# Optimization experiments

Measured on AMD Instinct MI355X. Metric: run time of the kernel, lower is better.

Reference implementation:

```python
import jax, jax.numpy as jnp
import numpy as np

EPS = 1e-6  # mmdet bbox_overlaps eps


def _nearest_bev(boxes7):
    # boxes7: [N, 7] = (x, y, z, dx, dy, dz, yaw). LiDARInstance3DBoxes.nearest_bev:
    # limit yaw to [-pi/2, pi/2) via limit_period(yaw, 0.5, pi); if |yaw| > pi/4 swap dx/dy,
    # then return axis-aligned (x1, y1, x2, y2).
    x, y = boxes7[:, 0], boxes7[:, 1]
    dx, dy = boxes7[:, 3], boxes7[:, 4]
    yaw = boxes7[:, 6]
    pi = jnp.float32(np.pi)
    normed = jnp.abs(yaw - jnp.floor(yaw / pi + 0.5) * pi)
    swap = normed > pi / 4
    w = jnp.where(swap, dy, dx)
    h = jnp.where(swap, dx, dy)
    return jnp.stack([x - w / 2, y - h / 2, x + w / 2, y + h / 2], axis=-1)


def _pairwise_iou(b):
    # b: [N, 4] x1y1x2y2 -> [N, N] IoU (mmdet bbox_overlaps, mode='iou')
    area = (b[:, 2] - b[:, 0]) * (b[:, 3] - b[:, 1])
    lt = jnp.maximum(b[:, None, :2], b[None, :, :2])
    rb = jnp.minimum(b[:, None, 2:], b[None, :, 2:])
    wh = jnp.clip(rb - lt, 0.0)
    inter = wh[..., 0] * wh[..., 1]
    union = jnp.maximum(area[:, None] + area[None, :] - inter, EPS)
    return inter / union


def setup_inputs() -> dict:
    key = jax.random.key(0)
    k1, k2, k3, k4, k5, k6 = jax.random.split(key, 6)
    B, A, C, H, W, box_dim = 2, 2, 10, 32, 32, 7
    N = H * W * A
    scores = jax.random.normal(k1, (B, A * C, H, W), jnp.float32)
    bbox_preds = jax.random.normal(k2, (B, A * box_dim, H, W), jnp.float32)
    pp_params = jax.random.normal(k3, (B, C * 3, H, W), jnp.float32)
    centers = jax.random.uniform(k4, (B, N, 3), jnp.float32, 0.0, 50.0)
    sizes = jax.random.uniform(k5, (B, N, 3), jnp.float32, 1.0, 5.0)
    yaw = jax.random.uniform(k6, (B, N, 1), jnp.float32, -np.pi, np.pi)
    decoded = jnp.concatenate([centers, sizes, yaw], axis=-1)  # [B, N, 7]
    return {"scores": scores, "bbox_preds": bbox_preds, "pp_params": pp_params, "decoded": decoded}


def reference(scores, bbox_preds, pp_params, decoded):
    B, AC, H, W = scores.shape
    N = decoded.shape[1]
    A = N // (H * W)
    C = AC // A
    # flatten_scores: (B,A,C,H,W) -> (B,H,W,A,C) -> (B, HWA, C)
    sc_f = scores.reshape(B, A, C, H, W).transpose(0, 3, 4, 1, 2).reshape(B, N, C)
    # flatten_pp: (B,C,3,H,W) -> (B,H,W,C,3), broadcast over A -> (B, HWA, C, 3)
    pp_hw = pp_params.reshape(B, C, 3, H, W).transpose(0, 3, 4, 1, 2)  # [B,H,W,C,3]
    pp_f = jnp.broadcast_to(pp_hw[:, :, :, None, :, :], (B, H, W, A, C, 3)).reshape(B, N, C, 3)
    # per-batch BEV IoU matrices
    bev = jax.vmap(_nearest_bev)(decoded[..., :7])        # [B, N, 4]
    iou = jax.vmap(_pairwise_iou)(bev)                    # [B, N, N]
    # per-class outer-product bias + row softmax + matmul with column softmax of scores
    p0 = pp_f[..., 0]                                     # [B, N, C]
    p1 = pp_f[..., 1]                                     # [B, N, C]
    bias = p0[:, :, None, :] * p1[:, None, :, :]          # [B, N, N, C]
    weight = jax.nn.softmax(iou[..., None] + bias, axis=2)  # softmax over keys (dim=1 of NxN)
    sm_sc = jax.nn.softmax(sc_f, axis=1)                  # softmax over N per class
    new_sc = jnp.einsum('bnmc,bmc->bnc', weight, sm_sc)   # [B, N, C]
    # un-flatten back to level layout: (B,H,W,A,C) -> (B, A*C, H, W)
    out_scores = new_sc.reshape(B, H, W, A, C).transpose(0, 3, 4, 1, 2).reshape(B, A * C, H, W)
    return out_scores, bbox_preds, pp_params
```

## Files before the change

### kernel.cpp

```cpp
#include <hip/hip_runtime.h>
#include <math.h>

#define Bz 2
#define Az 2
#define Cz 10
#define HWz 1024
#define Nz 2048
#define ACHW (Az*Cz*HWz)
#define NBBOX (Bz*Az*7*HWz)
#define NPP   (Bz*Cz*3*HWz)
#define EPSf 1e-6f
#define LOG2E 1.4426950408889634f

#if __has_builtin(__builtin_amdgcn_exp2f)
#define EXP2F(x) __builtin_amdgcn_exp2f(x)
#else
#define EXP2F(x) exp2f(x)
#endif
#if __has_builtin(__builtin_amdgcn_rcpf)
#define RCPF(x) __builtin_amdgcn_rcpf(x)
#else
#define RCPF(x) (1.0f/(x))
#endif

static __device__ __forceinline__ unsigned short f2bf(float x) {
    unsigned u = __builtin_bit_cast(unsigned, x);
    unsigned r = (u + 0x7fffu + ((u >> 16) & 1u)) >> 16;
    return (unsigned short)r;
}

#if __has_builtin(__builtin_amdgcn_update_dpp)
static __device__ __forceinline__ float wred(float x) {
    int t;
    t = __builtin_amdgcn_update_dpp(0, __builtin_bit_cast(int, x), 0x111, 0xf, 0xf, true);
    x += __builtin_bit_cast(float, t);
    t = __builtin_amdgcn_update_dpp(0, __builtin_bit_cast(int, x), 0x112, 0xf, 0xf, true);
    x += __builtin_bit_cast(float, t);
    t = __builtin_amdgcn_update_dpp(0, __builtin_bit_cast(int, x), 0x114, 0xf, 0xf, true);
    x += __builtin_bit_cast(float, t);
    t = __builtin_amdgcn_update_dpp(0, __builtin_bit_cast(int, x), 0x118, 0xf, 0xf, true);
    x += __builtin_bit_cast(float, t);
    t = __builtin_amdgcn_update_dpp(0, __builtin_bit_cast(int, x), 0x142, 0xa, 0xf, true);
    x += __builtin_bit_cast(float, t);
    t = __builtin_amdgcn_update_dpp(0, __builtin_bit_cast(int, x), 0x143, 0xc, 0xf, true);
    x += __builtin_bit_cast(float, t);
    return x;
}
#define WRED_LANE 63
#else
static __device__ __forceinline__ float wred(float x) {
    for (int off = 32; off > 0; off >>= 1) x += __shfl_down(x, off);
    return x;
}
#define WRED_LANE 0
#endif

static __device__ __forceinline__ float iou_e(float nx1,float ny1,float nx2,float ny2,float ar,
                                              float mx1,float my1,float mx2,float my2,float am) {
    float xx1 = fmaxf(nx1, mx1), yy1 = fmaxf(ny1, my1);
    float xx2 = fminf(nx2, mx2), yy2 = fminf(ny2, my2);
    float iw = fmaxf(xx2 - xx1, 0.f), ih = fmaxf(yy2 - yy1, 0.f);
    float inter = iw * ih;
    float uni = fmaxf(ar + am - inter, EPSf);
    return EXP2F(inter * LOG2E * RCPF(uni));
}

#define GL16(g, l) __builtin_amdgcn_global_load_lds( \
    (const __attribute__((address_space(1))) void*)(g), \
    (__attribute__((address_space(3))) void*)(l), 16, 0, 0)


__global__ __launch_bounds__(256) void k_pre(const float* __restrict__ scores,
                                             const float* __restrict__ bbox,
                                             const float* __restrict__ pp,
                                             const float* __restrict__ dec,
                                             float* __restrict__ out,
                                             float2* __restrict__ LT,
                                             float2* __restrict__ RB,
                                             uint2* __restrict__ GPQ) {
    int blk = blockIdx.x;
    int tid = threadIdx.x;

    if (blk < 240) {
        int i = blk * 256 + tid;
        if (i < NBBOX) out[Bz*ACHW + i] = bbox[i];
        if (i < NPP)   out[Bz*ACHW + NBBOX + i] = pp[i];
        return;
    }
    if (blk < 256) {
        int i = (blk - 240) * 256 + tid;
        const float* d = dec + i*7;
        float x = d[0], y = d[1], dx = d[3], dy = d[4], yaw = d[6];
        const float PI = 3.14159265358979323846f;
        float normed = fabsf(yaw - floorf(yaw/PI + 0.5f) * PI);
        bool swp = normed > PI * 0.25f;
        float w = swp ? dy : dx;
        float h = swp ? dx : dy;
        LT[i] = make_float2(x - 0.5f*w, y - 0.5f*h);
        RB[i] = make_float2(x + 0.5f*w, y + 0.5f*h);
        return;
    }
    __shared__ float wr4[4], ws4[4];
    __shared__ float SV[Nz];
    int wave = tid >> 6, lane = tid & 63;
    int bc = blk - 256;
    int b = bc / Cz, c = bc % Cz;
    const float* sbase = scores + b*ACHW;
    float vals[Nz/256];
    float mx = -INFINITY;
    #pragma unroll
    for (int j = 0; j < Nz/256; j++) {
        int n = tid + (j << 8);
        int a = n & 1, hw = n >> 1;
        float v = sbase[(a*Cz + c)*HWz + hw];
        vals[j] = v;
        mx = fmaxf(mx, v);
    }
    #pragma unroll
    for (int off = 32; off > 0; off >>= 1) mx = fmaxf(mx, __shfl_xor(mx, off));
    if (lane == 0) wr4[wave] = mx;
    __syncthreads();
    mx = fmaxf(fmaxf(wr4[0], wr4[1]), fmaxf(wr4[2], wr4[3]));
    float sum = 0.f;
    #pragma unroll
    for (int j = 0; j < Nz/256; j++) {
        float e = EXP2F((vals[j] - mx) * LOG2E);
        sum += e;
        SV[tid + (j << 8)] = e;
    }
    #pragma unroll
    for (int off = 32; off > 0; off >>= 1) sum += __shfl_xor(sum, off);
    if (lane == 0) ws4[wave] = sum;
    __syncthreads();
    float inv = 1.f / (ws4[0] + ws4[1] + ws4[2] + ws4[3]);
    const float* p1base = pp + b*Cz*3*HWz + (c*3 + 1)*HWz;
    uint2* gp = GPQ + (b*Cz + c)*HWz;
    #pragma unroll
    for (int k = 0; k < 4; k++) {
        int hm = tid + (k << 8);
        float q0 = SV[2*hm] * inv, q1 = SV[2*hm + 1] * inv;
        unsigned qq = (unsigned)f2bf(q0) | ((unsigned)f2bf(q1) << 16);
        float p1 = p1base[hm] * LOG2E;
        gp[hm] = make_uint2(__builtin_bit_cast(unsigned, p1), qq);
    }
}

__global__ __launch_bounds__(256, 4) void k_main(const float4* __restrict__ LT4,
                                                 const float4* __restrict__ RB4,
                                                 const uint2* __restrict__ GPQ,
                                                 const float* __restrict__ pp,
                                                 float* __restrict__ out) {
    __shared__ __align__(16) float4 SBuf[2][2][128];
    __shared__ __align__(16) uint2  SQb[2][2][640];
    __shared__ float SRED[2][2][40];

    int tid = threadIdx.x;
    int wave = tid >> 6, lane = tid & 63;
    int hl = wave >> 1;
    int s  = wave & 1;
    int bid = blockIdx.x;
    int b = bid >> 9;
    int g = bid & 511;
    int hn = (g << 1) + hl;
    int mb = s << 9;

    const float4* LTb = LT4 + (b << 10);
    const float4* RBb = RB4 + (b << 10);
    const uint2*  PQb = GPQ + b * (Cz * HWz);

    float4 bx = LTb[hn];
    float4 by = RBb[hn];
    float ar0 = (by.x - bx.x) * (by.y - bx.y);
    float ar1 = (by.z - bx.z) * (by.w - bx.w);

    float p0[Cz];
    const float* p0base = pp + b*(Cz*3*HWz) + hn;
    #pragma unroll
    for (int c = 0; c < Cz; c++) p0[c] = p0base[c * 3 * HWz];

    float l0[Cz], l1[Cz], a0[Cz], a1[Cz];
    #pragma unroll
    for (int c = 0; c < Cz; c++) { l0[c]=0.f; l1[c]=0.f; a0[c]=0.f; a1[c]=0.f; }

    auto stage = [&](int nb, int t) {
        int hbase = mb + (t << 6);
        if (hl) {
            GL16(LTb + hbase + lane, &SBuf[nb][s][0]);
            GL16(RBb + hbase + lane, &SBuf[nb][s][64]);
        } else {
            #pragma unroll
            for (int k = 0; k < 5; k++) {
                int p = (k << 6) + lane;
                int c = p >> 5;
                int hml2 = (p & 31) << 1;
                GL16(PQb + (c << 10) + hbase + hml2, &SQb[nb][s][k << 7]);
            }
        }
    };

    stage(0, 0);
    for (int it = 0; it < 8; ++it) {
        __syncthreads();
        int cur = it & 1;
        if (it < 7) stage(cur ^ 1, it + 1);

        float4 bl = SBuf[cur][s][lane];
        float4 br = SBuf[cur][s][64 + lane];
        float am0 = (br.x - bl.x) * (br.y - bl.y);
        float am1 = (br.z - bl.z) * (br.w - bl.w);
        float E00 = iou_e(bx.x,bx.y,by.x,by.y,ar0, bl.x,bl.y,br.x,br.y,am0);
        float E01 = iou_e(bx.x,bx.y,by.x,by.y,ar0, bl.z,bl.w,br.z,br.w,am1);
        float E10 = iou_e(bx.z,bx.w,by.z,by.w,ar1, bl.x,bl.y,br.x,br.y,am0);
        float E11 = iou_e(bx.z,bx.w,by.z,by.w,ar1, bl.z,bl.w,br.z,br.w,am1);
        float S0 = E00 + E01, S1 = E10 + E11;
        #pragma unroll
        for (int c = 0; c < Cz; c++) {
            uint2 pq = SQb[cur][s][(c << 6) + lane];
            float p1 = __builtin_bit_cast(float, pq.x);
            float q0 = __builtin_bit_cast(float, pq.y << 16);
            float q1 = __builtin_bit_cast(float, pq.y & 0xffff0000u);
            float F = EXP2F(p0[c] * p1);
            l0[c] = fmaf(F, S0, l0[c]);
            l1[c] = fmaf(F, S1, l1[c]);
            float t0 = fmaf(E01, q1, E00 * q0);
            float t1 = fmaf(E11, q1, E10 * q0);
            a0[c] = fmaf(F, t0, a0[c]);
            a1[c] = fmaf(F, t1, a1[c]);
        }
    }

    #pragma unroll
    for (int c = 0; c < Cz; c++) {
        l0[c] = wred(l0[c]); l1[c] = wred(l1[c]);
        a0[c] = wred(a0[c]); a1[c] = wred(a1[c]);
    }
    if (lane == WRED_LANE) {
        #pragma unroll
        for (int c = 0; c < Cz; c++) {
            SRED[hl][s][c]      = l0[c];
            SRED[hl][s][10 + c] = l1[c];
            SRED[hl][s][20 + c] = a0[c];
            SRED[hl][s][30 + c] = a1[c];
        }
    }
    __syncthreads();
    if (tid < 40) {
        int h   = tid >= 20 ? 1 : 0;
        int idx = tid - 20*h;
        int r   = idx >= 10 ? 1 : 0;
        int c   = idx - 10*r;
        float den = SRED[h][0][idx]      + SRED[h][1][idx];
        float num = SRED[h][0][20 + idx] + SRED[h][1][20 + idx];
        int hh = (g << 1) + h;
        out[b*ACHW + (r*Cz + c)*HWz + hh] = num * RCPF(den);
    }
}

extern "C" void kernel_launch(void* const* d_in, const int* in_sizes, int n_in,
                              void* d_out, int out_size, void* d_ws, size_t ws_size,
                              hipStream_t stream) {
    const float* scores = (const float*)d_in[0];
    const float* bbox   = (const float*)d_in[1];
    const float* pp     = (const float*)d_in[2];
    const float* dec    = (const float*)d_in[3];
    float* out = (float*)d_out;

    float2* LT = (float2*)d_ws;
    float2* RB = LT + (size_t)Bz*Nz;
    uint2*  PQ = (uint2*)(RB + (size_t)Bz*Nz);

    hipLaunchKernelGGL(k_pre,  dim3(276), dim3(256), 0, stream,
                       scores, bbox, pp, dec, out, LT, RB, PQ);
    hipLaunchKernelGGL(k_main, dim3(1024), dim3(256), 0, stream,
                       (const float4*)LT, (const float4*)RB, PQ, pp, out);
}
```

Baseline: 79.52 us.

## Drop LDS staging, load interleaved per-key class data directly; defer softmax normalisation

The main kernel no longer double-buffers box and class data through LDS with global_load_lds and barriers. Each lane now reads its key boxes and a class-interleaved record (five uint4 per key) straight from global memory. The score softmax skips the max subtraction and the per-element scaling, writing the sum Z to the workspace so the final output divides by it. This removes LDS traffic and barriers but adds scattered global loads, and dropping the max subtraction risks overflow for large scores.

```diff
diff --git a/kernel.cpp b/kernel.cpp
--- a/kernel.cpp
+++ b/kernel.cpp
@@ -65,10 +65,6 @@
     return EXP2F(inter * LOG2E * RCPF(uni));
 }
 
-#define GL16(g, l) __builtin_amdgcn_global_load_lds( \
-    (const __attribute__((address_space(1))) void*)(g), \
-    (__attribute__((address_space(3))) void*)(l), 16, 0, 0)
-
 
 __global__ __launch_bounds__(256) void k_pre(const float* __restrict__ scores,
                                              const float* __restrict__ bbox,
@@ -77,7 +73,8 @@
                                              float* __restrict__ out,
                                              float2* __restrict__ LT,
                                              float2* __restrict__ RB,
-                                             uint2* __restrict__ GPQ) {
+                                             uint2* __restrict__ PQ,
+                                             float* __restrict__ Z) {
     int blk = blockIdx.x;
     int tid = threadIdx.x;
 
@@ -100,58 +97,55 @@
         RB[i] = make_float2(x + 0.5f*w, y + 0.5f*h);
         return;
     }
-    __shared__ float wr4[4], ws4[4];
     __shared__ float SV[Nz];
+    __shared__ float ws4[4];
     int wave = tid >> 6, lane = tid & 63;
     int bc = blk - 256;
     int b = bc / Cz, c = bc % Cz;
-    const float* sbase = scores + b*ACHW;
-    float vals[Nz/256];
-    float mx = -INFINITY;
+    const float* sbase = scores + b*ACHW + c*HWz;
+    float sum = 0.f;
     #pragma unroll
     for (int j = 0; j < Nz/256; j++) {
         int n = tid + (j << 8);
         int a = n & 1, hw = n >> 1;
-        float v = sbase[(a*Cz + c)*HWz + hw];
-        vals[j] = v;
-        mx = fmaxf(mx, v);
-    }
-    #pragma unroll
-    for (int off = 32; off > 0; off >>= 1) mx = fmaxf(mx, __shfl_xor(mx, off));
-    if (lane == 0) wr4[wave] = mx;
-    __syncthreads();
-    mx = fmaxf(fmaxf(wr4[0], wr4[1]), fmaxf(wr4[2], wr4[3]));
-    float sum = 0.f;
-    #pragma unroll
-    for (int j = 0; j < Nz/256; j++) {
-        float e = EXP2F((vals[j] - mx) * LOG2E);
+        float e = EXP2F(sbase[a*(Cz*HWz) + hw] * LOG2E);
         sum += e;
-        SV[tid + (j << 8)] = e;
+        SV[n] = e;
     }
     #pragma unroll
     for (int off = 32; off > 0; off >>= 1) sum += __shfl_xor(sum, off);
     if (lane == 0) ws4[wave] = sum;
     __syncthreads();
-    float inv = 1.f / (ws4[0] + ws4[1] + ws4[2] + ws4[3]);
-    const float* p1base = pp + b*Cz*3*HWz + (c*3 + 1)*HWz;
-    uint2* gp = GPQ + (b*Cz + c)*HWz;
+    if (tid == 0) Z[b*Cz + c] = ws4[0] + ws4[1] + ws4[2] + ws4[3];
+    const float* p1base = pp + b*(Cz*3*HWz) + (c*3 + 1)*HWz;
+    uint2* gp = PQ + ((size_t)b << 10) * Cz + c;
     #pragma unroll
     for (int k = 0; k < 4; k++) {
         int hm = tid + (k << 8);
-        float q0 = SV[2*hm] * inv, q1 = SV[2*hm + 1] * inv;
-        unsigned qq = (unsigned)f2bf(q0) | ((unsigned)f2bf(q1) << 16);
+        unsigned qq = (unsigned)f2bf(SV[2*hm]) | ((unsigned)f2bf(SV[2*hm + 1]) << 16);
         float p1 = p1base[hm] * LOG2E;
-        gp[hm] = make_uint2(__builtin_bit_cast(unsigned, p1), qq);
-    }
-}
+        gp[(size_t)hm * Cz] = make_uint2(__builtin_bit_cast(unsigned, p1), qq);
+    }
+}
+
+#define PROC(P1BITS, QQ, c) { \
+    float p1_ = __builtin_bit_cast(float, (P1BITS)); \
+    float q0_ = __builtin_bit_cast(float, (QQ) << 16); \
+    float q1_ = __builtin_bit_cast(float, (QQ) & 0xffff0000u); \
+    float F_ = EXP2F(p0[c] * p1_); \
+    l0[c] = fmaf(F_, S0, l0[c]); \
+    l1[c] = fmaf(F_, S1, l1[c]); \
+    float t0_ = fmaf(E01, q1_, E00 * q0_); \
+    float t1_ = fmaf(E11, q1_, E10 * q0_); \
+    a0[c] = fmaf(F_, t0_, a0[c]); \
+    a1[c] = fmaf(F_, t1_, a1[c]); }
 
 __global__ __launch_bounds__(256, 4) void k_main(const float4* __restrict__ LT4,
                                                  const float4* __restrict__ RB4,
-                                                 const uint2* __restrict__ GPQ,
+                                                 const uint4* __restrict__ PQ4,
                                                  const float* __restrict__ pp,
+                                                 const float* __restrict__ Z,
                                                  float* __restrict__ out) {
-    __shared__ __align__(16) float4 SBuf[2][2][128];
-    __shared__ __align__(16) uint2  SQb[2][2][640];
     __shared__ float SRED[2][2][40];
 
     int tid = threadIdx.x;
@@ -166,7 +160,7 @@
 
     const float4* LTb = LT4 + (b << 10);
     const float4* RBb = RB4 + (b << 10);
-    const uint2*  PQb = GPQ + b * (Cz * HWz);
+    const uint4*  PQb = PQ4 + ((size_t)(b << 10)) * 5;
 
     float4 bx = LTb[hn];
     float4 by = RBb[hn];
@@ -182,30 +176,13 @@
     #pragma unroll
     for (int c = 0; c < Cz; c++) { l0[c]=0.f; l1[c]=0.f; a0[c]=0.f; a1[c]=0.f; }
 
-    auto stage = [&](int nb, int t) {
-        int hbase = mb + (t << 6);
-        if (hl) {
-            GL16(LTb + hbase + lane, &SBuf[nb][s][0]);
-            GL16(RBb + hbase + lane, &SBuf[nb][s][64]);
-        } else {
-            #pragma unroll
-            for (int k = 0; k < 5; k++) {
-                int p = (k << 6) + lane;
-                int c = p >> 5;
-                int hml2 = (p & 31) << 1;
-                GL16(PQb + (c << 10) + hbase + hml2, &SQb[nb][s][k << 7]);
-            }
-        }
-    };
-
-    stage(0, 0);
-    for (int it = 0; it < 8; ++it) {
-        __syncthreads();
-        int cur = it & 1;
-        if (it < 7) stage(cur ^ 1, it + 1);
-
-        float4 bl = SBuf[cur][s][lane];
-        float4 br = SBuf[cur][s][64 + lane];
+    for (int t = 0; t < 8; ++t) {
+        int hm = mb + (t << 6) + lane;
+        float4 bl = LTb[hm];
+        float4 br = RBb[hm];
+        const uint4* qp = PQb + (size_t)hm * 5;
+        uint4 r0 = qp[0], r1 = qp[1], r2 = qp[2], r3 = qp[3], r4 = qp[4];
+
         float am0 = (br.x - bl.x) * (br.y - bl.y);
         float am1 = (br.z - bl.z) * (br.w - bl.w);
         float E00 = iou_e(bx.x,bx.y,by.x,by.y,ar0, bl.x,bl.y,br.x,br.y,am0);
@@ -213,20 +190,12 @@
         float E10 = iou_e(bx.z,bx.w,by.z,by.w,ar1, bl.x,bl.y,br.x,br.y,am0);
         float E11 = iou_e(bx.z,bx.w,by.z,by.w,ar1, bl.z,bl.w,br.z,br.w,am1);
         float S0 = E00 + E01, S1 = E10 + E11;
-        #pragma unroll
-        for (int c = 0; c < Cz; c++) {
-            uint2 pq = SQb[cur][s][(c << 6) + lane];
-            float p1 = __builtin_bit_cast(float, pq.x);
-            float q0 = __builtin_bit_cast(float, pq.y << 16);
-            float q1 = __builtin_bit_cast(float, pq.y & 0xffff0000u);
-            float F = EXP2F(p0[c] * p1);
-            l0[c] = fmaf(F, S0, l0[c]);
-            l1[c] = fmaf(F, S1, l1[c]);
-            float t0 = fmaf(E01, q1, E00 * q0);
-            float t1 = fmaf(E11, q1, E10 * q0);
-            a0[c] = fmaf(F, t0, a0[c]);
-            a1[c] = fmaf(F, t1, a1[c]);
-        }
+
+        PROC(r0.x, r0.y, 0) PROC(r0.z, r0.w, 1)
+        PROC(r1.x, r1.y, 2) PROC(r1.z, r1.w, 3)
+        PROC(r2.x, r2.y, 4) PROC(r2.z, r2.w, 5)
+        PROC(r3.x, r3.y, 6) PROC(r3.z, r3.w, 7)
+        PROC(r4.x, r4.y, 8) PROC(r4.z, r4.w, 9)
     }
 
     #pragma unroll
@@ -249,8 +218,8 @@
         int idx = tid - 20*h;
         int r   = idx >= 10 ? 1 : 0;
         int c   = idx - 10*r;
-        float den = SRED[h][0][idx]      + SRED[h][1][idx];
-        float num = SRED[h][0][20 + idx] + SRED[h][1][20 + idx];
+        float den = (SRED[h][0][idx] + SRED[h][1][idx]) * Z[b*Cz + c];
+        float num =  SRED[h][0][20 + idx] + SRED[h][1][20 + idx];
         int hh = (g << 1) + h;
         out[b*ACHW + (r*Cz + c)*HWz + hh] = num * RCPF(den);
     }
@@ -268,9 +237,10 @@
     float2* LT = (float2*)d_ws;
     float2* RB = LT + (size_t)Bz*Nz;
     uint2*  PQ = (uint2*)(RB + (size_t)Bz*Nz);
+    float*  Z  = (float*)(PQ + (size_t)Bz*HWz*Cz);
 
     hipLaunchKernelGGL(k_pre,  dim3(276), dim3(256), 0, stream,
-                       scores, bbox, pp, dec, out, LT, RB, PQ);
+                       scores, bbox, pp, dec, out, LT, RB, PQ, Z);
     hipLaunchKernelGGL(k_main, dim3(1024), dim3(256), 0, stream,
-                       (const float4*)LT, (const float4*)RB, PQ, pp, out);
-}
+                       (const float4*)LT, (const float4*)RB, (const uint4*)PQ, pp, Z, out);
+}
```

Result: faster. 76.95 us (-3.2%).
